# Optimization experiments

Hardware: AMD Instinct MI355X
Metric: run time of the kernel (lower is better)

## Reference

```python
import jax, jax.numpy as jnp
import numpy as np

NS = 4      # num_streams
H = 8       # num_heads
E = 512     # embed_dim
HD = E // H # head_dim
SCALE = HD ** -0.5
LN_EPS = 1e-5


def _layer_norm(x, g, b):
    # x: [NS,B,S,E], g/b: [NS,E]
    m = jnp.mean(x, axis=-1, keepdims=True)
    v = jnp.mean((x - m) ** 2, axis=-1, keepdims=True)
    return (x - m) * jax.lax.rsqrt(v + LN_EPS) * g[:, None, None, :] + b[:, None, None, :]


def setup_inputs() -> dict:
    key = jax.random.key(0)
    ks = jax.random.split(key, 20)
    B, S = 4, 512
    f = lambda k, shp, s=0.02: (jax.random.normal(k, shp, dtype=jnp.float32) * s)
    inp = {
        "x0": jax.random.normal(ks[0], (B, S, E), dtype=jnp.float32),
        "x1": jax.random.normal(ks[1], (B, S, E), dtype=jnp.float32),
        "x2": jax.random.normal(ks[2], (B, S, E), dtype=jnp.float32),
        "x3": jax.random.normal(ks[3], (B, S, E), dtype=jnp.float32),
        # per-stream weights stacked on a leading NS axis; Linear stored as [in,out]
        "Wq": f(ks[4], (NS, E, E)),
        "Wk": f(ks[5], (NS, E, E)),
        "Wv": f(ks[6], (NS, E, E)),
        "Wo": f(ks[7], (NS, E, E)),
        "bo": jnp.zeros((NS, E), dtype=jnp.float32),
        "ln1_g": jnp.ones((NS, E), dtype=jnp.float32),
        "ln1_b": jnp.zeros((NS, E), dtype=jnp.float32),
        "ln2_g": jnp.ones((NS, E), dtype=jnp.float32),
        "ln2_b": jnp.zeros((NS, E), dtype=jnp.float32),
        "W1": f(ks[8], (NS, E, 4 * E)),
        "bf1": jnp.zeros((NS, 4 * E), dtype=jnp.float32),
        "W2": f(ks[9], (NS, 4 * E, E)),
        "bf2": jnp.zeros((NS, E), dtype=jnp.float32),
        "inter": jnp.eye(NS, dtype=jnp.float32) + 0.1 * jax.random.normal(ks[10], (NS, NS), dtype=jnp.float32),
    }
    return inp


def reference(x0, x1, x2, x3, Wq, Wk, Wv, Wo, bo, ln1_g, ln1_b, ln2_g, ln2_b,
              W1, bf1, W2, bf2, inter):
    x = jnp.stack([x0, x1, x2, x3], axis=0)  # [NS,B,S,E]
    B, S = x.shape[1], x.shape[2]

    def proj_heads(W):
        y = jnp.einsum('sbte,sef->sbtf', x, W)                 # [NS,B,S,E]
        return y.reshape(NS, B, S, H, HD).transpose(0, 1, 3, 2, 4)  # [NS,B,H,S,HD]

    q, k, v = proj_heads(Wq), proj_heads(Wk), proj_heads(Wv)

    # cross-stream scores for all (i,j) pairs, with interaction weight applied
    scores = jnp.einsum('ibhqd,jbhkd->ijbhqk', q, k) * SCALE    # [NS,NS,B,H,S,S]
    scores = scores * inter[:, :, None, None, None, None]
    attn = jax.nn.softmax(scores, axis=-1)                      # dropout is identity (eval)
    att = jnp.einsum('ijbhqk,jbhkd->ibhqd', attn, v) / NS       # [NS,B,H,S,HD]

    # concat heads -> [NS,B,S,E]
    mh = att.transpose(0, 1, 3, 2, 4).reshape(NS, B, S, E)
    # faithful to original: transpose(1,2).contiguous().view(B,S,E)
    mh = mh.transpose(0, 1, 3, 2).reshape(NS, B, S, E)

    proj = jnp.einsum('sbte,sef->sbtf', mh, Wo) + bo[:, None, None, :]
    r1 = _layer_norm(x + proj, ln1_g, ln1_b)

    h = jnp.einsum('sbte,sef->sbtf', r1, W1) + bf1[:, None, None, :]
    h = jax.nn.gelu(h, approximate=False)
    ffn = jnp.einsum('sbtf,sfe->sbte', h, W2) + bf2[:, None, None, :]

    out = _layer_norm(r1 + ffn, ln2_g, ln2_b)  # [NS,B,S,E]
    return (out[0], out[1], out[2], out[3])
```

## Files before the change

### kernel.cpp

```cpp
#include <hip/hip_runtime.h>
#include <hip/hip_bf16.h>

#define NSTREAM 4
#define BB 4
#define SEQ 512
#define EMB 512
#define NH 8
#define HD 64
#define FF 2048

typedef unsigned short u16;
typedef unsigned int u32;
typedef __attribute__((ext_vector_type(8))) short bf16x8;
typedef __attribute__((ext_vector_type(4))) float f32x4;
typedef __attribute__((ext_vector_type(16))) float f32x16;

__device__ __forceinline__ u16 f2bf(float x) {
  u32 u = __float_as_uint(x);
  return (u16)((u + 0x7fffu + ((u >> 16) & 1u)) >> 16);
}

__device__ __forceinline__ u32 pack_bf(float a, float b) {
  u32 r;
  asm("v_cvt_pk_bf16_f32 %0, %1, %2" : "=v"(r) : "v"(a), "v"(b));
  return r;
}

#define MFMA16(acc, a, b) \
  acc = __builtin_amdgcn_mfma_f32_16x16x32_bf16((a), (b), (acc), 0, 0, 0)
#define MFMA32(acc, a, b) \
  acc = __builtin_amdgcn_mfma_f32_32x32x16_bf16((a), (b), (acc), 0, 0, 0)

__device__ __forceinline__ void glds16(const void* g, void* l) {
  __builtin_amdgcn_global_load_lds(
      (const __attribute__((address_space(1))) void*)g,
      (__attribute__((address_space(3))) void*)l, 16, 0, 0);
}

__global__ __launch_bounds__(256) void k_transpose(const float* __restrict__ in,
                                                   u16* __restrict__ out,
                                                   int R, int C) {
  __shared__ float tile[32][33];
  size_t base = (size_t)blockIdx.z * R * C;
  int c0 = blockIdx.x * 32, r0 = blockIdx.y * 32;
  int tx = threadIdx.x & 31, ty = threadIdx.x >> 5;
#pragma unroll
  for (int i = 0; i < 32; i += 8)
    tile[ty + i][tx] = in[base + (size_t)(r0 + ty + i) * C + c0 + tx];
  __syncthreads();
#pragma unroll
  for (int i = 0; i < 32; i += 8)
    out[base + (size_t)(c0 + ty + i) * R + r0 + tx] = f2bf(tile[tx][ty + i]);
}

__global__ __launch_bounds__(256) void k_cvtx(const float* __restrict__ x0,
                                              const float* __restrict__ x1,
                                              const float* __restrict__ x2,
                                              const float* __restrict__ x3,
                                              u16* __restrict__ xb) {
  int s = blockIdx.y;
  const float* x = s == 0 ? x0 : s == 1 ? x1 : s == 2 ? x2 : x3;
  size_t idx = ((size_t)blockIdx.x * 256 + threadIdx.x) * 4;
  float4 v = *(const float4*)(x + idx);
  ushort4 o;
  o.x = f2bf(v.x); o.y = f2bf(v.y); o.z = f2bf(v.z); o.w = f2bf(v.w);
  *(ushort4*)(xb + (size_t)s * (BB * SEQ * EMB) + idx) = o;
}

template <int MODE>
__global__ __launch_bounds__(256) void k_gemm(
    const u16* __restrict__ A, const u16* __restrict__ B0,
    const u16* __restrict__ B1, const u16* __restrict__ B2,
    const float* __restrict__ bias,
    void* __restrict__ out0, void* __restrict__ out1, void* __restrict__ out2,
    int M, int N, int K) {
  __shared__ __align__(16) u16 lA[128 * 32];
  __shared__ __align__(16) u16 lB[128 * 32];

  int s, which;
  if (MODE == 0) { s = blockIdx.z / 3; which = blockIdx.z % 3; }
  else           { s = blockIdx.z; which = 0; }
  const u16* BT = (MODE == 0) ? (which == 0 ? B0 : (which == 1 ? B1 : B2)) : B0;

  const int tid = threadIdx.x;
  const int lane = tid & 63, w = tid >> 6;
  const int wm = w >> 1, wn = w & 1;
  const int lr = lane & 15, lg = lane >> 4;
  const int m0 = blockIdx.x * 128, n0 = blockIdx.y * 128;

  const u16* As = A + (size_t)s * M * K;
  const u16* Bs = BT + (size_t)s * N * K;

  f32x4 acc[4][4];
#pragma unroll
  for (int i = 0; i < 4; i++)
#pragma unroll
    for (int j = 0; j < 4; j++) acc[i][j] = f32x4{0.f, 0.f, 0.f, 0.f};

  const int r0 = tid >> 2;
  const int cb = (tid & 3) * 16;
  const int nkt = K >> 5;
  for (int kt = 0; kt < nkt; ++kt) {
    const int kof = kt * 32 + (cb >> 1);
#pragma unroll
    for (int slot = 0; slot < 2; ++slot) {
      int row = slot * 64 + r0;
      glds16(As + (size_t)(m0 + row) * K + kof, (char*)lA + slot * 4096 + w * 1024);
      glds16(Bs + (size_t)(n0 + row) * K + kof, (char*)lB + slot * 4096 + w * 1024);
    }
    __syncthreads();
    bf16x8 af[4], bfr[4];
#pragma unroll
    for (int mi = 0; mi < 4; mi++)
      af[mi] = *(const bf16x8*)&lA[(wm * 64 + mi * 16 + lr) * 32 + lg * 8];
#pragma unroll
    for (int ni = 0; ni < 4; ni++)
      bfr[ni] = *(const bf16x8*)&lB[(wn * 64 + ni * 16 + lr) * 32 + lg * 8];
#pragma unroll
    for (int mi = 0; mi < 4; mi++)
#pragma unroll
      for (int ni = 0; ni < 4; ni++) MFMA16(acc[mi][ni], af[mi], bfr[ni]);
    __syncthreads();
  }

  const int gmb = m0 + wm * 64, gnb = n0 + wn * 64;
#pragma unroll
  for (int mi = 0; mi < 4; mi++) {
#pragma unroll
    for (int ni = 0; ni < 4; ni++) {
#pragma unroll
      for (int r = 0; r < 4; r++) {
        int gm = gmb + mi * 16 + lg * 4 + r;
        int gn = gnb + ni * 16 + lr;
        float v = acc[mi][ni][r];
        if (MODE == 0) {
          int b = gm >> 9, t = gm & 511, hh = gn >> 6, d = gn & 63;
          if (which < 2) {
            u16* o = (u16*)(which == 0 ? out0 : out1);
            o[((((size_t)s * BB + b) * NH + hh) * SEQ + t) * HD + d] = f2bf(v);
          } else {
            int t2 = (t & ~12) | ((t & 4) << 1) | ((t & 8) >> 1);
            ((u16*)out2)[((((size_t)s * BB + b) * NH + hh) * HD + d) * SEQ + t2] = f2bf(v);
          }
        } else if (MODE == 1) {
          ((float*)out0)[((size_t)s * M + gm) * N + gn] = v + bias[(size_t)s * N + gn];
        } else {
          float xv = v + bias[(size_t)s * N + gn];
          float ge = 0.5f * xv * (1.0f + erff(xv * 0.70710678118654752f));
          ((u16*)out0)[((size_t)s * M + gm) * N + gn] = f2bf(ge);
        }
      }
    }
  }
}

__global__ __launch_bounds__(256) void k_attn(const u16* __restrict__ Q,
                                              const u16* __restrict__ Kb,
                                              const u16* __restrict__ Vt,
                                              const float* __restrict__ inter,
                                              u16* __restrict__ z) {
  const int tid = threadIdx.x, lane = tid & 63, w = tid >> 6;
  const int lq = lane & 31, hi = lane >> 5;
  const int qt = blockIdx.x * 4 + w;
  const int h = blockIdx.y;
  const int i = blockIdx.z >> 2, b = blockIdx.z & 3;

  const u16* Qbase = Q + ((((size_t)i * BB + b) * NH + h) * SEQ + qt * 32) * HD;
  bf16x8 qf[4];
#pragma unroll
  for (int c = 0; c < 4; c++)
    qf[c] = *(const bf16x8*)(Qbase + lq * HD + c * 16 + hi * 8);

  f32x16 acco0, acco1;
#pragma unroll
  for (int r = 0; r < 16; r++) { acco0[r] = 0.f; acco1[r] = 0.f; }

#define LOADK(dst, t)                                                        \
  _Pragma("unroll") for (int c = 0; c < 4; c++) dst[c] =                     \
      *(const bf16x8*)(Kp + ((t) * 32 + lq) * HD + c * 16 + hi * 8);
#define LOADV(dst, t)                                                        \
  _Pragma("unroll") for (int dt = 0; dt < 2; dt++) _Pragma("unroll")         \
      for (int m = 0; m < 2; m++) dst[dt * 2 + m] =                          \
          *(const bf16x8*)(Vp + (dt * 32 + lq) * SEQ + (t) * 32 + m * 16 + hi * 8);

#define PROCESS(kf, vf)                                                      \
  {                                                                          \
    f32x16 sv;                                                               \
    _Pragma("unroll") for (int r = 0; r < 16; r++) sv[r] = 0.f;              \
    MFMA32(sv, kf[0], qf[0]); MFMA32(sv, kf[1], qf[1]);                      \
    MFMA32(sv, kf[2], qf[2]); MFMA32(sv, kf[3], qf[3]);                      \
    _Pragma("unroll") for (int r = 0; r < 16; r++) sv[r] *= cij;             \
    float mxa = fmaxf(fmaxf(fmaxf(sv[0], sv[1]), fmaxf(sv[2], sv[3])),       \
                      fmaxf(fmaxf(sv[4], sv[5]), fmaxf(sv[6], sv[7])));      \
    float mxb = fmaxf(fmaxf(fmaxf(sv[8], sv[9]), fmaxf(sv[10], sv[11])),     \
                      fmaxf(fmaxf(sv[12], sv[13]), fmaxf(sv[14], sv[15])));  \
    float mx = fmaxf(mxa, mxb);                                              \
    mx = fmaxf(mx, __shfl_xor(mx, 32));                                      \
    if (__any(mx - m_run > 8.0f)) {                                          \
      float mnew = fmaxf(m_run, mx);                                         \
      float fac = __expf(m_run - mnew);                                      \
      _Pragma("unroll") for (int r = 0; r < 16; r++) {                       \
        accj0[r] *= fac; accj1[r] *= fac;                                    \
      }                                                                      \
      s_run *= fac; m_run = mnew;                                            \
    }                                                                        \
    _Pragma("unroll") for (int r = 0; r < 16; r++)                           \
        sv[r] = __expf(sv[r] - m_run);                                       \
    float sm = ((sv[0] + sv[1]) + (sv[2] + sv[3])) +                         \
               ((sv[4] + sv[5]) + (sv[6] + sv[7])) +                         \
               ((sv[8] + sv[9]) + (sv[10] + sv[11])) +                       \
               ((sv[12] + sv[13]) + (sv[14] + sv[15]));                      \
    sm += __shfl_xor(sm, 32);                                                \
    s_run += sm;                                                             \
    union { u32 u[4]; bf16x8 v; } pk1, pk2;                                  \
    pk1.u[0] = pack_bf(sv[0], sv[1]);  pk1.u[1] = pack_bf(sv[2], sv[3]);     \
    pk1.u[2] = pack_bf(sv[4], sv[5]);  pk1.u[3] = pack_bf(sv[6], sv[7]);     \
    pk2.u[0] = pack_bf(sv[8], sv[9]);  pk2.u[1] = pack_bf(sv[10], sv[11]);   \
    pk2.u[2] = pack_bf(sv[12], sv[13]); pk2.u[3] = pack_bf(sv[14], sv[15]);  \
    MFMA32(accj0, vf[0], pk1.v); MFMA32(accj0, vf[1], pk2.v);                \
    MFMA32(accj1, vf[2], pk1.v); MFMA32(accj1, vf[3], pk2.v);                \
  }

  for (int j = 0; j < NSTREAM; ++j) {
    const float cij = 0.125f * inter[i * NSTREAM + j];
    const u16* Kp = Kb + (((size_t)j * BB + b) * NH + h) * (SEQ * HD);
    const u16* Vp = Vt + (((size_t)j * BB + b) * NH + h) * (HD * SEQ);

    f32x16 accj0, accj1;
#pragma unroll
    for (int r = 0; r < 16; r++) { accj0[r] = 0.f; accj1[r] = 0.f; }
    float m_run = -3.0e38f, s_run = 0.f;

    bf16x8 kfA[4], vfA[4], kfB[4], vfB[4];
    LOADK(kfA, 0)
    LOADV(vfA, 0)
    for (int kp = 0; kp < 8; ++kp) {
      const int tB = 2 * kp + 1;
      LOADK(kfB, tB)
      LOADV(vfB, tB)
      PROCESS(kfA, vfA)
      if (kp < 7) {
        const int tA = 2 * kp + 2;
        LOADK(kfA, tA)
        LOADV(vfA, tA)
      }
      PROCESS(kfB, vfB)
    }

    float inv = 1.0f / s_run;
#pragma unroll
    for (int r = 0; r < 16; r++) {
      acco0[r] += accj0[r] * inv;
      acco1[r] += accj1[r] * inv;
    }
  }
#undef PROCESS
#undef LOADK
#undef LOADV

  u16* zp = z + (((size_t)(i * BB + b) * SEQ + h * HD) * EMB) + qt * 32 + lq;
#pragma unroll
  for (int r = 0; r < 16; r++) {
    int d0 = (r & 3) + 8 * (r >> 2) + 4 * hi;
    zp[(size_t)d0 * EMB] = f2bf(acco0[r] * 0.25f);
    zp[(size_t)(d0 + 32) * EMB] = f2bf(acco1[r] * 0.25f);
  }
}

__global__ __launch_bounds__(256) void k_ln1(
    const float* __restrict__ x0, const float* __restrict__ x1,
    const float* __restrict__ x2, const float* __restrict__ x3,
    const float* __restrict__ pr, const float* __restrict__ g,
    const float* __restrict__ be, float* __restrict__ r1f,
    u16* __restrict__ r1b) {
  const int rid = blockIdx.x;
  const int s = rid >> 11, bt = rid & 2047;
  const float* xs = s == 0 ? x0 : s == 1 ? x1 : s == 2 ? x2 : x3;
  const int tid = threadIdx.x, lane = tid & 63, w = tid >> 6;
  size_t ro = (size_t)rid * EMB;
  float v0 = xs[(size_t)bt * EMB + tid] + pr[ro + tid];
  float v1 = xs[(size_t)bt * EMB + tid + 256] + pr[ro + tid + 256];
  float sum = v0 + v1, sq = v0 * v0 + v1 * v1;
#pragma unroll
  for (int m = 1; m < 64; m <<= 1) { sum += __shfl_xor(sum, m); sq += __shfl_xor(sq, m); }
  __shared__ float ls[8];
  if (lane == 0) { ls[w] = sum; ls[4 + w] = sq; }
  __syncthreads();
  sum = ls[0] + ls[1] + ls[2] + ls[3];
  sq = ls[4] + ls[5] + ls[6] + ls[7];
  float mean = sum * (1.f / EMB);
  float var = sq * (1.f / EMB) - mean * mean;
  float inv = rsqrtf(var + 1e-5f);
  float o0 = (v0 - mean) * inv * g[s * EMB + tid] + be[s * EMB + tid];
  float o1 = (v1 - mean) * inv * g[s * EMB + tid + 256] + be[s * EMB + tid + 256];
  r1f[ro + tid] = o0; r1f[ro + tid + 256] = o1;
  r1b[ro + tid] = f2bf(o0); r1b[ro + tid + 256] = f2bf(o1);
}

__global__ __launch_bounds__(256) void k_ln2(
    const float* __restrict__ a, const float* __restrict__ bbuf,
    const float* __restrict__ g, const float* __restrict__ be,
    float* __restrict__ o) {
  const int rid = blockIdx.x;
  const int s = rid >> 11;
  const int tid = threadIdx.x, lane = tid & 63, w = tid >> 6;
  size_t ro = (size_t)rid * EMB;
  float v0 = a[ro + tid] + bbuf[ro + tid];
  float v1 = a[ro + tid + 256] + bbuf[ro + tid + 256];
  float sum = v0 + v1, sq = v0 * v0 + v1 * v1;
#pragma unroll
  for (int m = 1; m < 64; m <<= 1) { sum += __shfl_xor(sum, m); sq += __shfl_xor(sq, m); }
  __shared__ float ls[8];
  if (lane == 0) { ls[w] = sum; ls[4 + w] = sq; }
  __syncthreads();
  sum = ls[0] + ls[1] + ls[2] + ls[3];
  sq = ls[4] + ls[5] + ls[6] + ls[7];
  float mean = sum * (1.f / EMB);
  float var = sq * (1.f / EMB) - mean * mean;
  float inv = rsqrtf(var + 1e-5f);
  o[ro + tid] = (v0 - mean) * inv * g[s * EMB + tid] + be[s * EMB + tid];
  o[ro + tid + 256] = (v1 - mean) * inv * g[s * EMB + tid + 256] + be[s * EMB + tid + 256];
}

extern "C" void kernel_launch(void* const* d_in, const int* in_sizes, int n_in,
                              void* d_out, int out_size, void* d_ws, size_t ws_size,
                              hipStream_t stream) {
  const float* x0 = (const float*)d_in[0];
  const float* x1 = (const float*)d_in[1];
  const float* x2 = (const float*)d_in[2];
  const float* x3 = (const float*)d_in[3];
  const float* Wq = (const float*)d_in[4];
  const float* Wk = (const float*)d_in[5];
  const float* Wv = (const float*)d_in[6];
  const float* Wo = (const float*)d_in[7];
  const float* bo = (const float*)d_in[8];
  const float* ln1g = (const float*)d_in[9];
  const float* ln1b = (const float*)d_in[10];
  const float* ln2g = (const float*)d_in[11];
  const float* ln2b = (const float*)d_in[12];
  const float* W1 = (const float*)d_in[13];
  const float* bf1 = (const float*)d_in[14];
  const float* W2 = (const float*)d_in[15];
  const float* bf2 = (const float*)d_in[16];
  const float* inter = (const float*)d_in[17];
  float* out = (float*)d_out;

  char* ws = (char*)d_ws;
  size_t off = 0;
  auto alloc = [&](size_t bytes) {
    char* p = ws + off;
    off += (bytes + 255) & ~(size_t)255;
    return p;
  };
  const size_t TOK = (size_t)NSTREAM * BB * SEQ;
  u16* WqT = (u16*)alloc((size_t)NSTREAM * EMB * EMB * 2);
  u16* WkT = (u16*)alloc((size_t)NSTREAM * EMB * EMB * 2);
  u16* WvT = (u16*)alloc((size_t)NSTREAM * EMB * EMB * 2);
  u16* WoT = (u16*)alloc((size_t)NSTREAM * EMB * EMB * 2);
  u16* W1T = (u16*)alloc((size_t)NSTREAM * EMB * FF * 2);
  u16* W2T = (u16*)alloc((size_t)NSTREAM * FF * EMB * 2);
  u16* xb  = (u16*)alloc(TOK * EMB * 2);
  u16* Qb  = (u16*)alloc(TOK * EMB * 2);
  u16* Kbuf= (u16*)alloc(TOK * EMB * 2);
  u16* Vtb = (u16*)alloc(TOK * EMB * 2);
  float* tmp = (float*)alloc(TOK * EMB * 4);
  float* r1f = (float*)alloc(TOK * EMB * 4);
  u16* r1b = (u16*)alloc(TOK * EMB * 2);
  u16* hbuf = (u16*)alloc(TOK * FF * 2);

  dim3 blk(256);
  k_transpose<<<dim3(16, 16, 4), blk, 0, stream>>>(Wq, WqT, 512, 512);
  k_transpose<<<dim3(16, 16, 4), blk, 0, stream>>>(Wk, WkT, 512, 512);
  k_transpose<<<dim3(16, 16, 4), blk, 0, stream>>>(Wv, WvT, 512, 512);
  k_transpose<<<dim3(16, 16, 4), blk, 0, stream>>>(Wo, WoT, 512, 512);
  k_transpose<<<dim3(64, 16, 4), blk, 0, stream>>>(W1, W1T, 512, 2048);
  k_transpose<<<dim3(16, 64, 4), blk, 0, stream>>>(W2, W2T, 2048, 512);
  k_cvtx<<<dim3(1024, 4), blk, 0, stream>>>(x0, x1, x2, x3, xb);

  k_gemm<0><<<dim3(16, 4, 12), blk, 0, stream>>>(xb, WqT, WkT, WvT, nullptr,
                                                 Qb, Kbuf, Vtb, 2048, 512, 512);
  u16* zb = xb;
  k_attn<<<dim3(4, 8, 16), blk, 0, stream>>>(Qb, Kbuf, Vtb, inter, zb);
  k_gemm<1><<<dim3(16, 4, 4), blk, 0, stream>>>(zb, WoT, nullptr, nullptr, bo,
                                                tmp, nullptr, nullptr, 2048, 512, 512);
  k_ln1<<<dim3(8192), blk, 0, stream>>>(x0, x1, x2, x3, tmp, ln1g, ln1b, r1f, r1b);
  k_gemm<2><<<dim3(16, 16, 4), blk, 0, stream>>>(r1b, W1T, nullptr, nullptr, bf1,
                                                 hbuf, nullptr, nullptr, 2048, 2048, 512);
  k_gemm<1><<<dim3(16, 4, 4), blk, 0, stream>>>(hbuf, W2T, nullptr, nullptr, bf2,
                                                tmp, nullptr, nullptr, 2048, 512, 2048);
  k_ln2<<<dim3(8192), blk, 0, stream>>>(r1f, tmp, ln2g, ln2b, out);
}
```

Before: 414.9 us.

## Stage K/V tiles in swizzled LDS with async double-buffered loads in attention

The attention kernel no longer has each wave load K and V fragments straight from global memory. The block now cooperatively stages 64-token K/V tiles into double-buffered LDS using direct global-to-LDS loads, with waitcnt and barriers between stages. The QKV projection writes K and V in a pre-swizzled tiled layout so the LDS reads avoid bank conflicts, and the grid is flattened with a block-index swizzle to improve L2 locality. This targets redundant global traffic across the four waves of a block, at the cost of two barriers per tile and extra LDS use.

After: 366.6 us. 11.6% less time.

```diff
diff --git a/kernel.cpp b/kernel.cpp
--- a/kernel.cpp
+++ b/kernel.cpp
@@ -135,12 +135,18 @@
         float v = acc[mi][ni][r];
         if (MODE == 0) {
           int b = gm >> 9, t = gm & 511, hh = gn >> 6, d = gn & 63;
-          if (which < 2) {
-            u16* o = (u16*)(which == 0 ? out0 : out1);
-            o[((((size_t)s * BB + b) * NH + hh) * SEQ + t) * HD + d] = f2bf(v);
+          size_t base = (((size_t)s * BB + b) * NH + hh) * (SEQ * HD);
+          if (which == 0) {
+            ((u16*)out0)[base + (size_t)t * HD + d] = f2bf(v);
+          } else if (which == 1) {
+            int rr = t & 63;
+            ((u16*)out1)[base + (size_t)(t >> 6) * 4096 + rr * 64 +
+                         (d ^ ((rr & 7) << 3))] = f2bf(v);
           } else {
             int t2 = (t & ~12) | ((t & 4) << 1) | ((t & 8) >> 1);
-            ((u16*)out2)[((((size_t)s * BB + b) * NH + hh) * HD + d) * SEQ + t2] = f2bf(v);
+            int col = t2 & 63;
+            ((u16*)out2)[base + (size_t)(t2 >> 6) * 4096 + d * 64 +
+                         (col ^ ((d & 7) << 3))] = f2bf(v);
           }
         } else if (MODE == 1) {
           ((float*)out0)[((size_t)s * M + gm) * N + gn] = v + bias[(size_t)s * N + gn];
@@ -159,11 +165,18 @@
                                               const u16* __restrict__ Vt,
                                               const float* __restrict__ inter,
                                               u16* __restrict__ z) {
+  __shared__ __align__(16) u16 lK[2 * 4096];
+  __shared__ __align__(16) u16 lV[2 * 4096];
+
   const int tid = threadIdx.x, lane = tid & 63, w = tid >> 6;
   const int lq = lane & 31, hi = lane >> 5;
-  const int qt = blockIdx.x * 4 + w;
-  const int h = blockIdx.y;
-  const int i = blockIdx.z >> 2, b = blockIdx.z & 3;
+  const int bid = blockIdx.x;
+  const int sw = ((bid & 7) << 6) | (bid >> 3);
+  const int c_ = sw >> 6, w64 = sw & 63;
+  const int b = c_ >> 1;
+  const int h = ((c_ & 1) << 2) | (w64 >> 4);
+  const int i = (w64 >> 2) & 3;
+  const int qt = (w64 & 3) * 4 + w;
 
   const u16* Qbase = Q + ((((size_t)i * BB + b) * NH + h) * SEQ + qt * 32) * HD;
   bf16x8 qf[4];
@@ -175,88 +188,112 @@
 #pragma unroll
   for (int r = 0; r < 16; r++) { acco0[r] = 0.f; acco1[r] = 0.f; }
 
-#define LOADK(dst, t)                                                        \
-  _Pragma("unroll") for (int c = 0; c < 4; c++) dst[c] =                     \
-      *(const bf16x8*)(Kp + ((t) * 32 + lq) * HD + c * 16 + hi * 8);
-#define LOADV(dst, t)                                                        \
-  _Pragma("unroll") for (int dt = 0; dt < 2; dt++) _Pragma("unroll")         \
-      for (int m = 0; m < 2; m++) dst[dt * 2 + m] =                          \
-          *(const bf16x8*)(Vp + (dt * 32 + lq) * SEQ + (t) * 32 + m * 16 + hi * 8);
-
-#define PROCESS(kf, vf)                                                      \
-  {                                                                          \
-    f32x16 sv;                                                               \
-    _Pragma("unroll") for (int r = 0; r < 16; r++) sv[r] = 0.f;              \
-    MFMA32(sv, kf[0], qf[0]); MFMA32(sv, kf[1], qf[1]);                      \
-    MFMA32(sv, kf[2], qf[2]); MFMA32(sv, kf[3], qf[3]);                      \
-    _Pragma("unroll") for (int r = 0; r < 16; r++) sv[r] *= cij;             \
-    float mxa = fmaxf(fmaxf(fmaxf(sv[0], sv[1]), fmaxf(sv[2], sv[3])),       \
-                      fmaxf(fmaxf(sv[4], sv[5]), fmaxf(sv[6], sv[7])));      \
-    float mxb = fmaxf(fmaxf(fmaxf(sv[8], sv[9]), fmaxf(sv[10], sv[11])),     \
-                      fmaxf(fmaxf(sv[12], sv[13]), fmaxf(sv[14], sv[15])));  \
-    float mx = fmaxf(mxa, mxb);                                              \
-    mx = fmaxf(mx, __shfl_xor(mx, 32));                                      \
-    if (__any(mx - m_run > 8.0f)) {                                          \
-      float mnew = fmaxf(m_run, mx);                                         \
-      float fac = __expf(m_run - mnew);                                      \
-      _Pragma("unroll") for (int r = 0; r < 16; r++) {                       \
-        accj0[r] *= fac; accj1[r] *= fac;                                    \
-      }                                                                      \
-      s_run *= fac; m_run = mnew;                                            \
-    }                                                                        \
-    _Pragma("unroll") for (int r = 0; r < 16; r++)                           \
-        sv[r] = __expf(sv[r] - m_run);                                       \
-    float sm = ((sv[0] + sv[1]) + (sv[2] + sv[3])) +                         \
-               ((sv[4] + sv[5]) + (sv[6] + sv[7])) +                         \
-               ((sv[8] + sv[9]) + (sv[10] + sv[11])) +                       \
-               ((sv[12] + sv[13]) + (sv[14] + sv[15]));                      \
-    sm += __shfl_xor(sm, 32);                                                \
-    s_run += sm;                                                             \
-    union { u32 u[4]; bf16x8 v; } pk1, pk2;                                  \
-    pk1.u[0] = pack_bf(sv[0], sv[1]);  pk1.u[1] = pack_bf(sv[2], sv[3]);     \
-    pk1.u[2] = pack_bf(sv[4], sv[5]);  pk1.u[3] = pack_bf(sv[6], sv[7]);     \
-    pk2.u[0] = pack_bf(sv[8], sv[9]);  pk2.u[1] = pack_bf(sv[10], sv[11]);   \
-    pk2.u[2] = pack_bf(sv[12], sv[13]); pk2.u[3] = pack_bf(sv[14], sv[15]);  \
-    MFMA32(accj0, vf[0], pk1.v); MFMA32(accj0, vf[1], pk2.v);                \
-    MFMA32(accj1, vf[2], pk1.v); MFMA32(accj1, vf[3], pk2.v);                \
-  }
-
-  for (int j = 0; j < NSTREAM; ++j) {
-    const float cij = 0.125f * inter[i * NSTREAM + j];
-    const u16* Kp = Kb + (((size_t)j * BB + b) * NH + h) * (SEQ * HD);
-    const u16* Vp = Vt + (((size_t)j * BB + b) * NH + h) * (HD * SEQ);
-
-    f32x16 accj0, accj1;
-#pragma unroll
-    for (int r = 0; r < 16; r++) { accj0[r] = 0.f; accj1[r] = 0.f; }
-    float m_run = -3.0e38f, s_run = 0.f;
-
-    bf16x8 kfA[4], vfA[4], kfB[4], vfB[4];
-    LOADK(kfA, 0)
-    LOADV(vfA, 0)
-    for (int kp = 0; kp < 8; ++kp) {
-      const int tB = 2 * kp + 1;
-      LOADK(kfB, tB)
-      LOADV(vfB, tB)
-      PROCESS(kfA, vfA)
-      if (kp < 7) {
-        const int tA = 2 * kp + 2;
-        LOADK(kfA, tA)
-        LOADV(vfA, tA)
+#define STAGE(bufx, jj, dtt)                                                  \
+  {                                                                           \
+    size_t kvo = ((((size_t)(jj)) * BB + b) * NH + h) * 32768 + (dtt) * 4096; \
+    const u16* kb = Kb + kvo;                                                 \
+    const u16* vb = Vt + kvo;                                                 \
+    char* lkb = (char*)lK + (bufx) * 8192 + w * 1024;                         \
+    char* lvb = (char*)lV + (bufx) * 8192 + w * 1024;                         \
+    glds16(kb + tid * 8, lkb);                                                \
+    glds16(kb + 2048 + tid * 8, lkb + 4096);                                  \
+    glds16(vb + tid * 8, lvb);                                                \
+    glds16(vb + 2048 + tid * 8, lvb + 4096);                                  \
+  }
+
+#define PROCESS(tt)                                                           \
+  {                                                                           \
+    bf16x8 kf0, kf1, kf2, kf3, vf0, vf1, vf2, vf3;                            \
+    {                                                                         \
+      const char* kbp = (const char*)lK + buf * 8192;                         \
+      const int krow = (tt) * 32 + lq;                                        \
+      const int ksw = (krow & 7) << 4;                                        \
+      kf0 = *(const bf16x8*)(kbp + krow * 128 + ((0 * 32 + hi * 16) ^ ksw));  \
+      kf1 = *(const bf16x8*)(kbp + krow * 128 + ((1 * 32 + hi * 16) ^ ksw));  \
+      kf2 = *(const bf16x8*)(kbp + krow * 128 + ((2 * 32 + hi * 16) ^ ksw));  \
+      kf3 = *(const bf16x8*)(kbp + krow * 128 + ((3 * 32 + hi * 16) ^ ksw));  \
+      const char* vbp = (const char*)lV + buf * 8192;                         \
+      const int vs = (lq & 7) << 4;                                           \
+      vf0 = *(const bf16x8*)(vbp + lq * 128 + (((tt)*64 + 0*32 + hi*16) ^ vs));\
+      vf1 = *(const bf16x8*)(vbp + lq * 128 + (((tt)*64 + 1*32 + hi*16) ^ vs));\
+      vf2 = *(const bf16x8*)(vbp + (32+lq) * 128 + (((tt)*64 + 0*32 + hi*16) ^ vs));\
+      vf3 = *(const bf16x8*)(vbp + (32+lq) * 128 + (((tt)*64 + 1*32 + hi*16) ^ vs));\
+    }                                                                         \
+    f32x16 sv;                                                                \
+    _Pragma("unroll") for (int r = 0; r < 16; r++) sv[r] = 0.f;               \
+    MFMA32(sv, kf0, qf[0]); MFMA32(sv, kf1, qf[1]);                           \
+    MFMA32(sv, kf2, qf[2]); MFMA32(sv, kf3, qf[3]);                           \
+    _Pragma("unroll") for (int r = 0; r < 16; r++) sv[r] *= cij;              \
+    float mxa = fmaxf(fmaxf(fmaxf(sv[0], sv[1]), fmaxf(sv[2], sv[3])),        \
+                      fmaxf(fmaxf(sv[4], sv[5]), fmaxf(sv[6], sv[7])));       \
+    float mxb = fmaxf(fmaxf(fmaxf(sv[8], sv[9]), fmaxf(sv[10], sv[11])),      \
+                      fmaxf(fmaxf(sv[12], sv[13]), fmaxf(sv[14], sv[15])));   \
+    float mx = fmaxf(mxa, mxb);                                               \
+    mx = fmaxf(mx, __shfl_xor(mx, 32));                                       \
+    if (__any(mx - m_run > 8.0f)) {                                           \
+      float mnew = fmaxf(m_run, mx);                                          \
+      float fac = __expf(m_run - mnew);                                       \
+      _Pragma("unroll") for (int r = 0; r < 16; r++) {                        \
+        accj0[r] *= fac; accj1[r] *= fac;                                     \
+      }                                                                       \
+      s_run *= fac; m_run = mnew;                                             \
+    }                                                                         \
+    _Pragma("unroll") for (int r = 0; r < 16; r++)                            \
+        sv[r] = __expf(sv[r] - m_run);                                        \
+    float sm = ((sv[0] + sv[1]) + (sv[2] + sv[3])) +                          \
+               ((sv[4] + sv[5]) + (sv[6] + sv[7])) +                          \
+               ((sv[8] + sv[9]) + (sv[10] + sv[11])) +                        \
+               ((sv[12] + sv[13]) + (sv[14] + sv[15]));                       \
+    sm += __shfl_xor(sm, 32);                                                 \
+    s_run += sm;                                                              \
+    union { u32 u[4]; bf16x8 v; } pk1, pk2;                                   \
+    pk1.u[0] = pack_bf(sv[0], sv[1]);   pk1.u[1] = pack_bf(sv[2], sv[3]);     \
+    pk1.u[2] = pack_bf(sv[4], sv[5]);   pk1.u[3] = pack_bf(sv[6], sv[7]);     \
+    pk2.u[0] = pack_bf(sv[8], sv[9]);   pk2.u[1] = pack_bf(sv[10], sv[11]);   \
+    pk2.u[2] = pack_bf(sv[12], sv[13]); pk2.u[3] = pack_bf(sv[14], sv[15]);   \
+    MFMA32(accj0, vf0, pk1.v); MFMA32(accj0, vf1, pk2.v);                     \
+    MFMA32(accj1, vf2, pk1.v); MFMA32(accj1, vf3, pk2.v);                     \
+  }
+
+  f32x16 accj0, accj1;
+  float m_run = -3.0e38f, s_run = 0.f, cij = 0.f;
+  int buf = 0;
+
+  STAGE(0, 0, 0)
+  for (int r = 0; r < 32; ++r) {
+    const int j = r >> 3, dt = r & 7;
+    if (dt == 0) {
+      cij = 0.125f * inter[i * NSTREAM + j];
+#pragma unroll
+      for (int q = 0; q < 16; q++) { accj0[q] = 0.f; accj1[q] = 0.f; }
+      m_run = -3.0e38f;
+      s_run = 0.f;
+    }
+    if (r < 31) {
+      const int rn = r + 1;
+      STAGE(buf ^ 1, rn >> 3, rn & 7)
+      asm volatile("s_waitcnt vmcnt(4)" ::: "memory");
+    } else {
+      asm volatile("s_waitcnt vmcnt(0)" ::: "memory");
+    }
+    __builtin_amdgcn_s_barrier();
+    __builtin_amdgcn_sched_barrier(0);
+    PROCESS(0)
+    PROCESS(1)
+    __builtin_amdgcn_sched_barrier(0);
+    __builtin_amdgcn_s_barrier();
+    if (dt == 7) {
+      float inv = 1.0f / s_run;
+#pragma unroll
+      for (int q = 0; q < 16; q++) {
+        acco0[q] += accj0[q] * inv;
+        acco1[q] += accj1[q] * inv;
       }
-      PROCESS(kfB, vfB)
     }
-
-    float inv = 1.0f / s_run;
-#pragma unroll
-    for (int r = 0; r < 16; r++) {
-      acco0[r] += accj0[r] * inv;
-      acco1[r] += accj1[r] * inv;
-    }
+    buf ^= 1;
   }
 #undef PROCESS
-#undef LOADK
-#undef LOADV
+#undef STAGE
 
   u16* zp = z + (((size_t)(i * BB + b) * SEQ + h * HD) * EMB) + qt * 32 + lq;
 #pragma unroll
@@ -380,7 +417,7 @@
   k_gemm<0><<<dim3(16, 4, 12), blk, 0, stream>>>(xb, WqT, WkT, WvT, nullptr,
                                                  Qb, Kbuf, Vtb, 2048, 512, 512);
   u16* zb = xb;
-  k_attn<<<dim3(4, 8, 16), blk, 0, stream>>>(Qb, Kbuf, Vtb, inter, zb);
+  k_attn<<<dim3(512), blk, 0, stream>>>(Qb, Kbuf, Vtb, inter, zb);
   k_gemm<1><<<dim3(16, 4, 4), blk, 0, stream>>>(zb, WoT, nullptr, nullptr, bo,
                                                 tmp, nullptr, nullptr, 2048, 512, 512);
   k_ln1<<<dim3(8192), blk, 0, stream>>>(x0, x1, x2, x3, tmp, ln1g, ln1b, r1f, r1b);
```
